# Performance work log

Measured on AMD Instinct MI355X. Metric: run time of the kernel, lower is better.

The kernel has to match this reference:

```python
import jax, jax.numpy as jnp
import numpy as np

IN_C, OUT_C, K, STRIDE, PAD = 128, 256, 3, 1, 1
B, H, W = 32, 56, 56


def setup_inputs() -> dict:
    key = jax.random.key(0)
    kx, kw = jax.random.split(key)
    x = jax.random.normal(kx, (B, IN_C, H, W), dtype=jnp.float32)
    # He init, matching torch.randn(out_c,in_c,k,k) * (2/(in_c*k*k))**0.5
    Wk = jax.random.normal(kw, (OUT_C, IN_C, K, K), dtype=jnp.float32) * (2.0 / (IN_C * K * K)) ** 0.5
    b = jnp.zeros((OUT_C,), dtype=jnp.float32)
    return {"x": x, "Wk": Wk, "b": b}


def reference(x, Wk, b):
    # Same math as the module's zero-pad + im2col + GEMM pipeline,
    # expressed as a direct convolution (implicit GEMM).
    out = jax.lax.conv_general_dilated(
        x, Wk,
        window_strides=(STRIDE, STRIDE),
        padding=[(PAD, PAD), (PAD, PAD)],
        dimension_numbers=("NCHW", "OIHW", "NCHW"),
    )
    return out + b[None, :, None, None]
```

## Files before the change

### kernel.cpp

```cpp
#include <hip/hip_runtime.h>

#define IN_C  128
#define OUT_C 256
#define HIMG  56
#define WIMG  56
#define BIMG  32
#define HW    (HIMG * WIMG)
#define KW    1152

#define BM    128
#define TH    4
#define XROWS 6
#define XCOLS 58
#define NPIXT (XROWS * XCOLS)
#define XS_SH (NPIXT * 32)
#define AS_SH 4096
#define NT    36
#define WT_TILES 39
#define XCH   (NPIXT * 4)

#define NX_BYTES 27557888u

typedef __attribute__((ext_vector_type(8))) short short8;
typedef __attribute__((ext_vector_type(4))) float float4_;

__device__ __forceinline__ unsigned short f32_to_bf16_rne(float f) {
    unsigned u = __builtin_bit_cast(unsigned, f);
    u += 0x7FFFu + ((u >> 16) & 1u);
    return (unsigned short)(u >> 16);
}

#define ASYNC16(g, l) __builtin_amdgcn_global_load_lds( \
    (const __attribute__((address_space(1))) unsigned int*)(g), \
    (__attribute__((address_space(3))) unsigned int*)(l), 16, 0, 0)

__global__ __launch_bounds__(256) void x_to_nhwc(
    const float* __restrict__ x, unsigned short* __restrict__ nx)
{
    __shared__ unsigned short T[128][58];
    const int b  = blockIdx.x;
    const int hp = blockIdx.y;
    unsigned short* dst = nx + (size_t)(b * 58 + hp) * 58 * 128;

    if (hp == 0 || hp == 57) {
        for (int i = threadIdx.x; i < 58 * 128; i += 256) dst[i] = 0;
        return;
    }
    const int h = hp - 1;
    for (int e = threadIdx.x; e < 128 * 56; e += 256) {
        int c = e / 56, w = e - c * 56;
        T[c][w] = f32_to_bf16_rne(x[(size_t)(b * IN_C + c) * HW + h * WIMG + w]);
    }
    __syncthreads();
    for (int e = threadIdx.x; e < 58 * 128; e += 256) {
        int wp = e >> 7, c = e & 127;
        dst[wp * 128 + c] = (wp == 0 || wp == 57) ? (unsigned short)0 : T[c][wp - 1];
    }
}

__global__ void repack_w(const float* __restrict__ Wk, unsigned short* __restrict__ Wt) {
    int idx = blockIdx.x * 256 + threadIdx.x;
    if (idx >= 2 * WT_TILES * 4096) return;
    int half = idx / (WT_TILES * 4096);
    int rem  = idx - half * (WT_TILES * 4096);
    int t    = rem >> 12;
    int win  = rem & 4095;
    int oc   = win >> 5;
    int c    = (win >> 3) & 3;
    int j    = win & 7;
    unsigned short v = 0;
    if (t < NT) {
        int icq = t / 9, r = t - icq * 9;
        int s  = c ^ ((oc >> 1) & 3);
        int ic = icq * 32 + s * 8 + j;
        v = f32_to_bf16_rne(Wk[(size_t)(half * 128 + oc) * KW + ic * 9 + r]);
    }
    Wt[idx] = v;
}

__global__ __launch_bounds__(256, 2) void conv_gemm(
    const unsigned short* __restrict__ nx,
    const unsigned short* __restrict__ Wt,
    const float* __restrict__ bias, float* __restrict__ out)
{
    __shared__ __align__(16) unsigned short As[4 * AS_SH];
    __shared__ __align__(16) unsigned short Xs[2 * XS_SH];

    const int tid  = threadIdx.x;
    const int lane = tid & 63;
    const int wid  = tid >> 6;
    const int bx   = blockIdx.x;
    const int b    = bx / 14;
    const int h0   = (bx - b * 14) * TH;
    const int half = blockIdx.y;

    const int wm = (wid >> 1) * 64;
    const int wn = (wid & 1) * 112;
    const int q  = lane >> 4;

    int lp0[7], outoff[7];
    #pragma unroll
    for (int ni = 0; ni < 7; ++ni) {
        int nl  = wn + ni * 16 + (lane & 15);
        int ht_ = nl / 56;
        int wt_ = nl - ht_ * 56;
        lp0[ni]    = (ht_ + 1) * XCOLS + (wt_ + 1);
        outoff[ni] = (h0 + ht_) * WIMG + wt_;
    }

    int aoff[4];
    #pragma unroll
    for (int mi = 0; mi < 4; ++mi) {
        int row = wm + mi * 16 + (lane & 15);
        aoff[mi] = row * 32 + ((q ^ ((row >> 1) & 3)) * 8);
    }

    int xgo[6];
    #pragma unroll
    for (int i = 0; i < 6; ++i) {
        int C = wid * 348 + i * 64 + lane;
        if (C >= XCH) C = XCH - 1;
        int p = C >> 2, c = C & 3;
        int row  = p / XCOLS;
        int colw = p - row * XCOLS;
        int s = c ^ ((p >> 1) & 3);
        xgo[i] = ((b * 58 + h0 + row) * 58 + colw) * 256 + s * 16;
    }
    const char* nxc = (const char*)nx;
    const char* wtc = (const char*)Wt + (size_t)half * WT_TILES * 8192
                    + (wid * 2) * 1024 + lane * 16;

    float4_ acc[4][7];
    #pragma unroll
    for (int mi = 0; mi < 4; ++mi)
        #pragma unroll
        for (int ni = 0; ni < 7; ++ni) acc[mi][ni] = (float4_)0.0f;

    auto stage_x = [&](int icq1, int bufX1) {
        #pragma unroll
        for (int i = 0; i < 5; ++i)
            ASYNC16(nxc + xgo[i] + icq1 * 64,
                    &Xs[bufX1 * XS_SH + (wid * 348 + i * 64) * 8]);
        if (lane < 28)
            ASYNC16(nxc + xgo[5] + icq1 * 64,
                    &Xs[bufX1 * XS_SH + (wid * 348 + 5 * 64) * 8]);
    };
    auto stage_a = [&](int tile) {
        const char* src = wtc + (size_t)tile * 8192;
        unsigned short* dst = &As[(tile & 3) * AS_SH + (wid * 2) * 512];
        ASYNC16(src, dst);
        ASYNC16(src + 1024, dst + 512);
    };

    stage_x(0, 0);
    stage_a(0); stage_a(1); stage_a(2);

    for (int t = 0; t < NT; ++t) {
        const int icq = t / 9;
        const int r   = t - icq * 9;

        if (r >= 1 && r <= 3) asm volatile("s_waitcnt vmcnt(10)" ::: "memory");
        else                  asm volatile("s_waitcnt vmcnt(4)"  ::: "memory");
        __builtin_amdgcn_s_barrier();
        asm volatile("" ::: "memory");

        const unsigned short* Ab = &As[(t & 3) * AS_SH];
        const unsigned short* Xb = &Xs[(icq & 1) * XS_SH];
        const int doff = (r / 3 - 1) * XCOLS + (r - (r / 3) * 3 - 1);

        short8 afr[4], bfr[7];
        #pragma unroll
        for (int mi = 0; mi < 4; ++mi) afr[mi] = *(const short8*)&Ab[aoff[mi]];
        #pragma unroll
        for (int ni = 0; ni < 7; ++ni) {
            int lp   = lp0[ni] + doff;
            int slot = q ^ ((lp >> 1) & 3);
            bfr[ni]  = *(const short8*)&Xb[lp * 32 + slot * 8];
        }

        stage_a(t + 3);
        if (r == 0) stage_x(icq + 1, (icq + 1) & 1);

        __builtin_amdgcn_s_setprio(1);
        #pragma unroll
        for (int mi = 0; mi < 4; ++mi)
            #pragma unroll
            for (int ni = 0; ni < 7; ++ni)
                acc[mi][ni] = __builtin_amdgcn_mfma_f32_16x16x32_bf16(
                    afr[mi], bfr[ni], acc[mi][ni], 0, 0, 0);
        __builtin_amdgcn_s_setprio(0);
    }

    const int rowg = (lane >> 4) * 4;
    const int oc0  = half * BM;
    #pragma unroll
    for (int mi = 0; mi < 4; ++mi) {
        #pragma unroll
        for (int v = 0; v < 4; ++v) {
            const int oc = oc0 + wm + mi * 16 + rowg + v;
            const float bv = bias[oc];
            float* obase = out + (size_t)(b * OUT_C + oc) * HW;
            #pragma unroll
            for (int ni = 0; ni < 7; ++ni)
                obase[outoff[ni]] = acc[mi][ni][v] + bv;
        }
    }
}

extern "C" void kernel_launch(void* const* d_in, const int* in_sizes, int n_in,
                              void* d_out, int out_size, void* d_ws, size_t ws_size,
                              hipStream_t stream) {
    (void)in_sizes; (void)n_in; (void)out_size; (void)ws_size;
    const float* x    = (const float*)d_in[0];
    const float* Wk   = (const float*)d_in[1];
    const float* bias = (const float*)d_in[2];
    float* out        = (float*)d_out;

    unsigned short* nx = (unsigned short*)d_ws;
    unsigned short* Wt = (unsigned short*)((char*)d_ws + NX_BYTES);

    x_to_nhwc<<<dim3(BIMG, 58), dim3(256), 0, stream>>>(x, nx);
    repack_w<<<dim3((2 * WT_TILES * 4096 + 255) / 256), dim3(256), 0, stream>>>(Wk, Wt);
    conv_gemm<<<dim3(BIMG * (HIMG / TH), OUT_C / BM), dim3(256), 0, stream>>>(nx, Wt, bias, out);
}
```

Measured before the change: 201.1 us.

## Load weight fragments directly into registers, drop LDS staging and per-tap barriers

```diff
diff --git a/kernel.cpp b/kernel.cpp
--- a/kernel.cpp
+++ b/kernel.cpp
@@ -14,14 +14,13 @@
 #define XCOLS 58
 #define NPIXT (XROWS * XCOLS)
 #define XS_SH (NPIXT * 32)
-#define AS_SH 4096
+#define XCH   (NPIXT * 4)
 #define NT    36
-#define WT_TILES 39
-#define XCH   (NPIXT * 4)
 
 #define NX_BYTES 27557888u
 
 typedef __attribute__((ext_vector_type(8))) short short8;
+typedef __attribute__((ext_vector_type(4))) short short4_;
 typedef __attribute__((ext_vector_type(4))) float float4_;
 
 __device__ __forceinline__ unsigned short f32_to_bf16_rne(float f) {
@@ -58,24 +57,25 @@
     }
 }
 
-__global__ void repack_w(const float* __restrict__ Wk, unsigned short* __restrict__ Wt) {
-    int idx = blockIdx.x * 256 + threadIdx.x;
-    if (idx >= 2 * WT_TILES * 4096) return;
-    int half = idx / (WT_TILES * 4096);
-    int rem  = idx - half * (WT_TILES * 4096);
-    int t    = rem >> 12;
-    int win  = rem & 4095;
-    int oc   = win >> 5;
-    int c    = (win >> 3) & 3;
-    int j    = win & 7;
-    unsigned short v = 0;
-    if (t < NT) {
+__global__ __launch_bounds__(256) void repack_w(
+    const float* __restrict__ Wk, unsigned short* __restrict__ Wt)
+{
+    __shared__ float L[8 * KW];
+    const int oc0 = blockIdx.x * 8;
+    for (int i = threadIdx.x; i < 8 * KW; i += 256)
+        L[i] = Wk[(size_t)oc0 * KW + i];
+    __syncthreads();
+    for (int e = threadIdx.x; e < 2304; e += 256) {
+        int jg = e & 1, q = (e >> 1) & 3, oc = (e >> 3) & 7, t = e >> 6;
         int icq = t / 9, r = t - icq * 9;
-        int s  = c ^ ((oc >> 1) & 3);
-        int ic = icq * 32 + s * 8 + j;
-        v = f32_to_bf16_rne(Wk[(size_t)(half * 128 + oc) * KW + ic * 9 + r]);
-    }
-    Wt[idx] = v;
+        short4_ v;
+        #pragma unroll
+        for (int jj = 0; jj < 4; ++jj) {
+            int ic = icq * 32 + q * 8 + jg * 4 + jj;
+            v[jj] = (short)f32_to_bf16_rne(L[oc * KW + ic * 9 + r]);
+        }
+        *(short4_*)&Wt[(size_t)(((t * 256 + oc0 + oc) * 4 + q) * 8 + jg * 4)] = v;
+    }
 }
 
 __global__ __launch_bounds__(256, 2) void conv_gemm(
@@ -83,7 +83,6 @@
     const unsigned short* __restrict__ Wt,
     const float* __restrict__ bias, float* __restrict__ out)
 {
-    __shared__ __align__(16) unsigned short As[4 * AS_SH];
     __shared__ __align__(16) unsigned short Xs[2 * XS_SH];
 
     const int tid  = threadIdx.x;
@@ -108,12 +107,8 @@
         outoff[ni] = (h0 + ht_) * WIMG + wt_;
     }
 
-    int aoff[4];
-    #pragma unroll
-    for (int mi = 0; mi < 4; ++mi) {
-        int row = wm + mi * 16 + (lane & 15);
-        aoff[mi] = row * 32 + ((q ^ ((row >> 1) & 3)) * 8);
-    }
+    const char* wbase = (const char*)Wt
+        + ((size_t)(half * BM + wm + (lane & 15)) * 4 + q) * 16;
 
     int xgo[6];
     #pragma unroll
@@ -127,8 +122,6 @@
         xgo[i] = ((b * 58 + h0 + row) * 58 + colw) * 256 + s * 16;
     }
     const char* nxc = (const char*)nx;
-    const char* wtc = (const char*)Wt + (size_t)half * WT_TILES * 8192
-                    + (wid * 2) * 1024 + lane * 16;
 
     float4_ acc[4][7];
     #pragma unroll
@@ -145,51 +138,55 @@
             ASYNC16(nxc + xgo[5] + icq1 * 64,
                     &Xs[bufX1 * XS_SH + (wid * 348 + 5 * 64) * 8]);
     };
-    auto stage_a = [&](int tile) {
-        const char* src = wtc + (size_t)tile * 8192;
-        unsigned short* dst = &As[(tile & 3) * AS_SH + (wid * 2) * 512];
-        ASYNC16(src, dst);
-        ASYNC16(src + 1024, dst + 512);
-    };
+
+    short8 areg[3][4];
+    #define LOADA(T, S)                                                        \
+        {                                                                      \
+            _Pragma("unroll")                                                  \
+            for (int mi = 0; mi < 4; ++mi)                                     \
+                areg[S][mi] = *(const short8*)(wbase + (size_t)(T) * 16384     \
+                                               + mi * 1024);                   \
+        }
 
     stage_x(0, 0);
-    stage_a(0); stage_a(1); stage_a(2);
-
-    for (int t = 0; t < NT; ++t) {
-        const int icq = t / 9;
-        const int r   = t - icq * 9;
-
-        if (r >= 1 && r <= 3) asm volatile("s_waitcnt vmcnt(10)" ::: "memory");
-        else                  asm volatile("s_waitcnt vmcnt(4)"  ::: "memory");
+    LOADA(0, 0);
+    LOADA(1, 1);
+
+    #pragma unroll
+    for (int icq = 0; icq < 4; ++icq) {
+        asm volatile("s_waitcnt vmcnt(0)" ::: "memory");
         __builtin_amdgcn_s_barrier();
         asm volatile("" ::: "memory");
 
-        const unsigned short* Ab = &As[(t & 3) * AS_SH];
         const unsigned short* Xb = &Xs[(icq & 1) * XS_SH];
-        const int doff = (r / 3 - 1) * XCOLS + (r - (r / 3) * 3 - 1);
-
-        short8 afr[4], bfr[7];
-        #pragma unroll
-        for (int mi = 0; mi < 4; ++mi) afr[mi] = *(const short8*)&Ab[aoff[mi]];
-        #pragma unroll
-        for (int ni = 0; ni < 7; ++ni) {
-            int lp   = lp0[ni] + doff;
-            int slot = q ^ ((lp >> 1) & 3);
-            bfr[ni]  = *(const short8*)&Xb[lp * 32 + slot * 8];
-        }
-
-        stage_a(t + 3);
-        if (r == 0) stage_x(icq + 1, (icq + 1) & 1);
-
-        __builtin_amdgcn_s_setprio(1);
-        #pragma unroll
-        for (int mi = 0; mi < 4; ++mi)
+
+        #pragma unroll
+        for (int r = 0; r < 9; ++r) {
+            const int t    = icq * 9 + r;
+            const int doff = (r / 3 - 1) * XCOLS + (r % 3 - 1);
+
+            short8 bfr[7];
             #pragma unroll
-            for (int ni = 0; ni < 7; ++ni)
-                acc[mi][ni] = __builtin_amdgcn_mfma_f32_16x16x32_bf16(
-                    afr[mi], bfr[ni], acc[mi][ni], 0, 0, 0);
-        __builtin_amdgcn_s_setprio(0);
-    }
+            for (int ni = 0; ni < 7; ++ni) {
+                int lp   = lp0[ni] + doff;
+                int slot = q ^ ((lp >> 1) & 3);
+                bfr[ni]  = *(const short8*)&Xb[lp * 32 + slot * 8];
+            }
+
+            if (t + 2 < NT) LOADA(t + 2, (t + 2) % 3);
+            if (r == 0 && icq < 3) stage_x(icq + 1, (icq + 1) & 1);
+
+            __builtin_amdgcn_s_setprio(1);
+            #pragma unroll
+            for (int mi = 0; mi < 4; ++mi)
+                #pragma unroll
+                for (int ni = 0; ni < 7; ++ni)
+                    acc[mi][ni] = __builtin_amdgcn_mfma_f32_16x16x32_bf16(
+                        areg[t % 3][mi], bfr[ni], acc[mi][ni], 0, 0, 0);
+            __builtin_amdgcn_s_setprio(0);
+        }
+    }
+    #undef LOADA
 
     const int rowg = (lane >> 4) * 4;
     const int oc0  = half * BM;
@@ -220,6 +217,6 @@
     unsigned short* Wt = (unsigned short*)((char*)d_ws + NX_BYTES);
 
     x_to_nhwc<<<dim3(BIMG, 58), dim3(256), 0, stream>>>(x, nx);
-    repack_w<<<dim3((2 * WT_TILES * 4096 + 255) / 256), dim3(256), 0, stream>>>(Wk, Wt);
+    repack_w<<<dim3(OUT_C / 8), dim3(256), 0, stream>>>(Wk, Wt);
     conv_gemm<<<dim3(BIMG * (HIMG / TH), OUT_C / BM), dim3(256), 0, stream>>>(nx, Wt, bias, out);
 }
```

Measured after the change: 272.2 us. 35.4% more time.
